# Kernel tuning notes

Measured on AMD Instinct MI355X. Metric: run time of the kernel, lower is better.

The kernel has to match this reference:

```python
import jax, jax.numpy as jnp
import numpy as np

TOP_K = 2

def setup_inputs() -> dict:
    key = jax.random.key(0)
    k1, k2, k3, k4 = jax.random.split(key, 4)
    B, S, D, E = 4, 4096, 2048, 8
    x = jax.random.normal(k1, (B, S, D), dtype=jnp.float32)
    w_g = jax.random.normal(k2, (E, D), dtype=jnp.float32) * (1.0 / np.sqrt(D))
    w_noise = jax.random.normal(k3, (E, D), dtype=jnp.float32) * (1.0 / np.sqrt(D))
    eps = jax.random.normal(k4, (B, S, E), dtype=jnp.float32)
    return {"x": x, "w_g": w_g, "w_noise": w_noise, "eps": eps}

def reference(x, w_g, w_noise, eps):
    # gate logits: [B, S, E]
    logits = jnp.einsum('bsd,ed->bse', x, w_g)
    # noisy top-k: logits += softplus(x @ w_noise.T) * eps
    noise = jax.nn.softplus(jnp.einsum('bsd,ed->bse', x, w_noise)) * eps
    logits = logits + noise
    top_k_logits, top_k_indices = jax.lax.top_k(logits, TOP_K)
    return (top_k_logits, top_k_indices)
```

## Files before the change

kernel.cpp:

```cpp
#include <hip/hip_runtime.h>
#include <math.h>

#define TOKENS 16384
#define DIM 2048
#define NE 8
#define BLOCK 1024
#define GRID 256
#define NCHUNK 8

template <int CTRL>
__device__ __forceinline__ float dpp_mov(float v) {
    return __int_as_float(__builtin_amdgcn_update_dpp(
        0, __float_as_int(v), CTRL, 0xf, 0xf, true));
}
#define DPP_XOR1 0xB1
#define DPP_XOR2 0x4E
#define DPP_XOR8 0x128

__device__ __forceinline__ void stage16(const float* g, float* l) {
    __builtin_amdgcn_global_load_lds(
        (const __attribute__((address_space(1))) void*)g,
        (__attribute__((address_space(3))) void*)l, 16, 0, 0);
}

#define FMA_BODY(XBUF, KC)                                         \
    {                                                              \
        const int kk = (KC);                                       \
        _Pragma("unroll")                                          \
        for (int r = 0; r < 16; ++r) {                             \
            const float4 w = wl4[r * (DIM / 4) + kk * 64 + lane];  \
            _Pragma("unroll")                                      \
            for (int t = 0; t < 4; ++t) {                          \
                float a = V[r * 4 + t];                            \
                a = fmaf(XBUF[t].x, w.x, a);                       \
                a = fmaf(XBUF[t].y, w.y, a);                       \
                a = fmaf(XBUF[t].z, w.z, a);                       \
                a = fmaf(XBUF[t].w, w.w, a);                       \
                V[r * 4 + t] = a;                                  \
            }                                                      \
        }                                                          \
    }
#define REFILL(XBUF, KC)                                           \
    {                                                              \
        const int kk = (KC);                                       \
        _Pragma("unroll")                                          \
        for (int t = 0; t < 4; ++t)                                \
            XBUF[t] = x4[(t0 + t) * (DIM / 4) + kk * 64 + lane];   \
    }

__launch_bounds__(BLOCK, 4)
__global__ void router_kernel(const float* __restrict__ x,
                              const float* __restrict__ w_g,
                              const float* __restrict__ w_noise,
                              const float* __restrict__ eps,
                              float* __restrict__ out)
{
    __shared__ float wlds[16 * DIM];

    const int tid  = threadIdx.x;
    const int lane = tid & 63;
    const int wv   = tid >> 6;
    const int t0   = (blockIdx.x * 16 + wv) * 4;
    const int off  = wv & 3;

    int c[8];
    #pragma unroll
    for (int j = 0; j < 8; ++j)
        c[j] = ((j + off) & 3) + ((j >= 4) ? 4 : 0);

    const float* wrow = (wv < 8) ? (w_g + wv * DIM) : (w_noise + (wv - 8) * DIM);
    float* lrow = &wlds[wv * DIM];

    #pragma unroll
    for (int i = 0; i < 4; ++i)
        stage16(wrow + i * 256 + lane * 4, lrow + i * 256);

    const float4* x4 = (const float4*)x;
    float4 xvA[4], xvB[4];
    #pragma unroll
    for (int t = 0; t < 4; ++t) xvA[t] = x4[(t0 + t) * (DIM / 4) + c[0] * 64 + lane];
    #pragma unroll
    for (int t = 0; t < 4; ++t) xvB[t] = x4[(t0 + t) * (DIM / 4) + c[1] * 64 + lane];

    float my_eps = 0.f;
    if (lane < 32) my_eps = eps[t0 * NE + lane];

    __syncthreads();

    #pragma unroll
    for (int i = 0; i < 4; ++i)
        stage16(wrow + 1024 + i * 256 + lane * 4, lrow + 1024 + i * 256);

    const float4* wl4 = (const float4*)wlds;

    float V[64];
    #pragma unroll
    for (int v = 0; v < 64; ++v) V[v] = 0.f;

    FMA_BODY(xvA, c[0]); REFILL(xvA, c[2]);
    FMA_BODY(xvB, c[1]); REFILL(xvB, c[3]);
    FMA_BODY(xvA, c[2]); REFILL(xvA, c[4]);
    FMA_BODY(xvB, c[3]); REFILL(xvB, c[5]);

    __syncthreads();

    FMA_BODY(xvA, c[4]); REFILL(xvA, c[6]);
    FMA_BODY(xvB, c[5]); REFILL(xvB, c[7]);
    FMA_BODY(xvA, c[6]);
    FMA_BODY(xvB, c[7]);

    #pragma unroll
    for (int j = 0; j < 32; ++j) {
        const float A = V[2 * j], B = V[2 * j + 1];
        const float As = dpp_mov<DPP_XOR1>(A);
        const float Bs = dpp_mov<DPP_XOR1>(B);
        V[j] = (lane & 1) ? (B + Bs) : (A + As);
    }
    #pragma unroll
    for (int j = 0; j < 16; ++j) {
        const float A = V[2 * j], B = V[2 * j + 1];
        const float As = dpp_mov<DPP_XOR2>(A);
        const float Bs = dpp_mov<DPP_XOR2>(B);
        V[j] = (lane & 2) ? (B + Bs) : (A + As);
    }
    #pragma unroll
    for (int j = 0; j < 8; ++j) {
        const float A = V[2 * j], B = V[2 * j + 1];
        const float As = __shfl_xor(A, 4, 64);
        const float Bs = __shfl_xor(B, 4, 64);
        V[j] = (lane & 4) ? (B + Bs) : (A + As);
    }
    #pragma unroll
    for (int j = 0; j < 4; ++j) {
        const float A = V[2 * j], B = V[2 * j + 1];
        const float As = dpp_mov<DPP_XOR8>(A);
        const float Bs = dpp_mov<DPP_XOR8>(B);
        V[j] = (lane & 8) ? (B + Bs) : (A + As);
    }
    #pragma unroll
    for (int j = 0; j < 2; ++j) {
        const float A = V[2 * j], B = V[2 * j + 1];
        const float As = __shfl_xor(A, 16, 64);
        const float Bs = __shfl_xor(B, 16, 64);
        V[j] = (lane & 16) ? (B + Bs) : (A + As);
    }
    {
        const float A = V[0], B = V[1];
        const float As = __shfl_xor(A, 32, 64);
        const float Bs = __shfl_xor(B, 32, 64);
        V[0] = (lane & 32) ? (B + Bs) : (A + As);
    }
    const float mine = V[0];

    const float other = __shfl_xor(mine, 32, 64);

    if (lane < 32) {
        const int e = lane >> 2;
        const int t = lane & 3;
        const int tok = t0 + t;

        const float ev = __shfl(my_eps, (t << 3) | e, 64);

        const float nv = other;
        const float sp = fmaxf(nv, 0.f) + log1pf(expf(-fabsf(nv)));
        const float logit = fmaf(sp, ev, mine);

        float v1 = logit, v2 = -INFINITY;
        int   i1 = e,     i2 = 7;
        #pragma unroll
        for (int sm = 2; sm <= 4; ++sm) {
            const int m = 1 << sm;
            const float ov1 = __shfl_xor(v1, m, 64);
            const float ov2 = __shfl_xor(v2, m, 64);
            const int   oi1 = __shfl_xor(i1, m, 64);
            const int   oi2 = __shfl_xor(i2, m, 64);
            const bool firstA = (v1 > ov1) || (v1 == ov1 && i1 < oi1);
            const float nv1 = firstA ? v1  : ov1;
            const int   ni1 = firstA ? i1  : oi1;
            const float ca  = firstA ? ov1 : v1;
            const int   cia = firstA ? oi1 : i1;
            const float cb  = firstA ? v2  : ov2;
            const int   cib = firstA ? i2  : oi2;
            const bool secondA = (ca > cb) || (ca == cb && cia < cib);
            v1 = nv1; i1 = ni1;
            v2 = secondA ? ca : cb;
            i2 = secondA ? cia : cib;
        }

        if (e == 0) {
            *(float2*)&out[2 * tok] = make_float2(v1, v2);
            *(float2*)&out[2 * TOKENS + 2 * tok] = make_float2((float)i1, (float)i2);
        }
    }
}

extern "C" void kernel_launch(void* const* d_in, const int* in_sizes, int n_in,
                              void* d_out, int out_size, void* d_ws, size_t ws_size,
                              hipStream_t stream) {
    const float* x       = (const float*)d_in[0];
    const float* w_g     = (const float*)d_in[1];
    const float* w_noise = (const float*)d_in[2];
    const float* eps     = (const float*)d_in[3];
    float* out = (float*)d_out;

    router_kernel<<<GRID, BLOCK, 0, stream>>>(x, w_g, w_noise, eps, out);
}
```

Baseline: 32.27 us.

## Read gate weights directly from global memory instead of staging in LDS

Removes the LDS staging of both weight matrices and the block barriers. Each wave now loads w_g and w_noise float4s straight from global memory, relying on the cache since the 128KB of weights is shared by all waves. Blocks shrink to 256 threads with a 4x larger grid, and the chunk rotation is rewritten as a loop. This trades LDS fills and syncs for repeated global/L2 weight reads per wave and higher load-latency exposure.

```diff
diff --git a/kernel.cpp b/kernel.cpp
--- a/kernel.cpp
+++ b/kernel.cpp
@@ -4,9 +4,8 @@
 #define TOKENS 16384
 #define DIM 2048
 #define NE 8
-#define BLOCK 1024
-#define GRID 256
-#define NCHUNK 8
+#define BLOCK 256
+#define GRID 1024
 
 template <int CTRL>
 __device__ __forceinline__ float dpp_mov(float v) {
@@ -17,35 +16,36 @@
 #define DPP_XOR2 0x4E
 #define DPP_XOR8 0x128
 
-__device__ __forceinline__ void stage16(const float* g, float* l) {
-    __builtin_amdgcn_global_load_lds(
-        (const __attribute__((address_space(1))) void*)g,
-        (__attribute__((address_space(3))) void*)l, 16, 0, 0);
-}
-
-#define FMA_BODY(XBUF, KC)                                         \
-    {                                                              \
-        const int kk = (KC);                                       \
-        _Pragma("unroll")                                          \
-        for (int r = 0; r < 16; ++r) {                             \
-            const float4 w = wl4[r * (DIM / 4) + kk * 64 + lane];  \
-            _Pragma("unroll")                                      \
-            for (int t = 0; t < 4; ++t) {                          \
-                float a = V[r * 4 + t];                            \
-                a = fmaf(XBUF[t].x, w.x, a);                       \
-                a = fmaf(XBUF[t].y, w.y, a);                       \
-                a = fmaf(XBUF[t].z, w.z, a);                       \
-                a = fmaf(XBUF[t].w, w.w, a);                       \
-                V[r * 4 + t] = a;                                  \
-            }                                                      \
-        }                                                          \
+#define FMA_BODY(XBUF, KC)                                              \
+    {                                                                   \
+        const int kk = (KC);                                            \
+        _Pragma("unroll")                                               \
+        for (int r = 0; r < 8; ++r) {                                   \
+            const float4 wg = g4[r * 512 + kk * 64 + lane];             \
+            const float4 wn = n4[r * 512 + kk * 64 + lane];             \
+            _Pragma("unroll")                                           \
+            for (int t = 0; t < 4; ++t) {                               \
+                float a = V[r * 4 + t];                                 \
+                a = fmaf(XBUF[t].x, wg.x, a);                           \
+                a = fmaf(XBUF[t].y, wg.y, a);                           \
+                a = fmaf(XBUF[t].z, wg.z, a);                           \
+                a = fmaf(XBUF[t].w, wg.w, a);                           \
+                V[r * 4 + t] = a;                                       \
+                float b = V[32 + r * 4 + t];                            \
+                b = fmaf(XBUF[t].x, wn.x, b);                           \
+                b = fmaf(XBUF[t].y, wn.y, b);                           \
+                b = fmaf(XBUF[t].z, wn.z, b);                           \
+                b = fmaf(XBUF[t].w, wn.w, b);                           \
+                V[32 + r * 4 + t] = b;                                  \
+            }                                                           \
+        }                                                               \
     }
-#define REFILL(XBUF, KC)                                           \
-    {                                                              \
-        const int kk = (KC);                                       \
-        _Pragma("unroll")                                          \
-        for (int t = 0; t < 4; ++t)                                \
-            XBUF[t] = x4[(t0 + t) * (DIM / 4) + kk * 64 + lane];   \
+#define REFILL(XBUF, KC)                                                \
+    {                                                                   \
+        const int kk = (KC);                                            \
+        _Pragma("unroll")                                               \
+        for (int t = 0; t < 4; ++t)                                     \
+            XBUF[t] = x4[(t0 + t) * (DIM / 4) + kk * 64 + lane];        \
     }
 
 __launch_bounds__(BLOCK, 4)
@@ -55,59 +55,36 @@
                               const float* __restrict__ eps,
                               float* __restrict__ out)
 {
-    __shared__ float wlds[16 * DIM];
-
     const int tid  = threadIdx.x;
     const int lane = tid & 63;
     const int wv   = tid >> 6;
-    const int t0   = (blockIdx.x * 16 + wv) * 4;
-    const int off  = wv & 3;
-
-    int c[8];
-    #pragma unroll
-    for (int j = 0; j < 8; ++j)
-        c[j] = ((j + off) & 3) + ((j >= 4) ? 4 : 0);
-
-    const float* wrow = (wv < 8) ? (w_g + wv * DIM) : (w_noise + (wv - 8) * DIM);
-    float* lrow = &wlds[wv * DIM];
-
-    #pragma unroll
-    for (int i = 0; i < 4; ++i)
-        stage16(wrow + i * 256 + lane * 4, lrow + i * 256);
+    const int t0   = (blockIdx.x * 4 + wv) * 4;
+    const int off  = (wv & 3) * 2;
 
     const float4* x4 = (const float4*)x;
+    const float4* g4 = (const float4*)w_g;
+    const float4* n4 = (const float4*)w_noise;
+
     float4 xvA[4], xvB[4];
-    #pragma unroll
-    for (int t = 0; t < 4; ++t) xvA[t] = x4[(t0 + t) * (DIM / 4) + c[0] * 64 + lane];
-    #pragma unroll
-    for (int t = 0; t < 4; ++t) xvB[t] = x4[(t0 + t) * (DIM / 4) + c[1] * 64 + lane];
+    REFILL(xvA, off);
+    REFILL(xvB, (1 + off) & 7);
 
     float my_eps = 0.f;
     if (lane < 32) my_eps = eps[t0 * NE + lane];
-
-    __syncthreads();
-
-    #pragma unroll
-    for (int i = 0; i < 4; ++i)
-        stage16(wrow + 1024 + i * 256 + lane * 4, lrow + 1024 + i * 256);
-
-    const float4* wl4 = (const float4*)wlds;
 
     float V[64];
     #pragma unroll
     for (int v = 0; v < 64; ++v) V[v] = 0.f;
 
-    FMA_BODY(xvA, c[0]); REFILL(xvA, c[2]);
-    FMA_BODY(xvB, c[1]); REFILL(xvB, c[3]);
-    FMA_BODY(xvA, c[2]); REFILL(xvA, c[4]);
-    FMA_BODY(xvB, c[3]); REFILL(xvB, c[5]);
-
-    __syncthreads();
-
-    FMA_BODY(xvA, c[4]); REFILL(xvA, c[6]);
-    FMA_BODY(xvB, c[5]); REFILL(xvB, c[7]);
-    FMA_BODY(xvA, c[6]);
-    FMA_BODY(xvB, c[7]);
+    #pragma unroll
+    for (int i = 0; i < 8; i += 2) {
+        const int kA = (i + off) & 7;
+        const int kB = (i + 1 + off) & 7;
+        FMA_BODY(xvA, kA);
+        if (i + 2 < 8) REFILL(xvA, (i + 2 + off) & 7);
+        FMA_BODY(xvB, kB);
+        if (i + 3 < 8) REFILL(xvB, (i + 3 + off) & 7);
+    }
 
     #pragma unroll
     for (int j = 0; j < 32; ++j) {
```

After: 36.28 us. 12.4% more time.
